# Optimization experiments

Hardware: AMD Instinct MI355X
Metric: run time of the kernel (lower is better)

## Reference

```python
import jax, jax.numpy as jnp
import numpy as np

T, B, I, H = 2048, 2048, 1, 20


def setup_inputs() -> dict:
    key = jax.random.key(0)
    k0, k1, k2, k3, k4 = jax.random.split(key, 5)
    x = jax.random.normal(k0, (T, B, I), dtype=jnp.float32)
    # Concatenated gate weights in order [f, i, o, c]; equivalent to the
    # module's 8 separate nn.Linear layers (wf/uf, wi/ui, wo/uo, wc/uc).
    W = jax.random.normal(k1, (4 * H, I), dtype=jnp.float32) * 0.2
    U = jax.random.normal(k2, (4 * H, H), dtype=jnp.float32) * 0.2
    bw = jax.random.normal(k3, (4 * H,), dtype=jnp.float32) * 0.1  # Linear(w*) biases
    bu = jax.random.normal(k4, (4 * H,), dtype=jnp.float32) * 0.1  # Linear(u*) biases
    return {"x": x, "W": W, "U": U, "bw": bw, "bu": bu}


def reference(x, W, U, bw, bu):
    h_dim = U.shape[1]
    b = x.shape[1]
    # Precompute input projections for all timesteps: (T, B, 4H).
    # Original adds both Linear biases (bw from w*, bu from u*) plus zero b*.
    xz = jnp.einsum('tbi,gi->tbg', x, W) + bw + bu

    def step(carry, xz_t):
        h, c = carry
        z = xz_t + h @ U.T  # (B, 4H)
        f, i, o, g = jnp.split(z, 4, axis=-1)
        f = jax.nn.sigmoid(f)
        i = jax.nn.sigmoid(i)
        o = jax.nn.sigmoid(o)
        g = jnp.tanh(g)
        c = f * c + i * g
        h = o * jnp.tanh(c)
        return (h, c), h

    h0 = jnp.zeros((b, h_dim), dtype=x.dtype)
    c0 = jnp.zeros((b, h_dim), dtype=x.dtype)
    (h_last, c_last), h_seq = jax.lax.scan(step, (h0, c0), xz)
    return h_seq, h_last, c_last
```

## Files before the change

kernel.cpp:

```cpp
#include <hip/hip_runtime.h>
#include <cstddef>


constexpr int T = 2048;
constexpr int B = 2048;
constexpr int H = 20;
constexpr int GR = 3;
constexpr int SLOTS = 4;
constexpr int ROW = 36;
constexpr int CHUNK = 16;
constexpr int NCH = T / CHUNK;

typedef float f2   __attribute__((ext_vector_type(2)));
typedef float f4ma __attribute__((ext_vector_type(4), may_alias));

__device__ __forceinline__ float rcp_f(float v) { return __builtin_amdgcn_rcpf(v); }
__device__ __forceinline__ float ex2(float v)   { return __builtin_amdgcn_exp2f(v); }

__global__ __launch_bounds__(64, 1)
void lstm_w7(const float* __restrict__ xg, const float* __restrict__ Wg,
             const float* __restrict__ Ug, const float* __restrict__ bwg,
             const float* __restrict__ bug, float* __restrict__ out) {
  __shared__ float hx[2][SLOTS * ROW];

  const int tid = threadIdx.x;
  const int bl  = tid / H;
  const int j   = tid % H;
  const int bg0 = blockIdx.x * GR + bl;
  const bool st = (bl < GR) && (bg0 < B);
  const int bgi = (bg0 < B) ? bg0 : (B - 1);

  constexpr float K1 = 1.44269504f;

  f2 u01[H], u23[H], w01, w23, b01, b23;
#pragma unroll
  for (int k = 0; k < H; ++k) {
    u01[k].x = Ug[(0 * H + j) * H + k] * (-K1);
    u01[k].y = Ug[(1 * H + j) * H + k] * (-K1);
    u23[k].x = Ug[(2 * H + j) * H + k] * (-K1);
    u23[k].y = Ug[(3 * H + j) * H + k] * (2.0f * K1);
  }
  w01.x = Wg[0 * H + j] * (-K1);   w01.y = Wg[1 * H + j] * (-K1);
  w23.x = Wg[2 * H + j] * (-K1);   w23.y = Wg[3 * H + j] * (2.0f * K1);
  b01.x = (bwg[0 * H + j] + bug[0 * H + j]) * (-K1);
  b01.y = (bwg[1 * H + j] + bug[1 * H + j]) * (-K1);
  b23.x = (bwg[2 * H + j] + bug[2 * H + j]) * (-K1);
  b23.y = (bwg[3 * H + j] + bug[3 * H + j]) * (2.0f * K1);

  for (int q = tid; q < 2 * SLOTS * ROW; q += 64) (&hx[0][0])[q] = 0.f;
  __builtin_amdgcn_wave_barrier();

  float xv[CHUNK];
#pragma unroll
  for (int s = 0; s < CHUNK; ++s) xv[s] = xg[(size_t)s * B + bgi];

  float c2 = 0.f;
  float hn = 0.f;
  float* outp = out + (size_t)bgi * H + j;
  constexpr size_t OS = (size_t)B * H;

  const int hbase = bl * ROW;

  for (int ch = 0; ch < NCH; ++ch) {
#pragma unroll
    for (int s = 0; s < CHUNK; ++s) {
      const int p = s & 1;
      __builtin_amdgcn_wave_barrier();
      const f4ma* hp = reinterpret_cast<const f4ma*>(&hx[p][hbase]);
      const f4ma v0 = hp[0], v1 = hp[1], v2 = hp[2], v3 = hp[3], v4 = hp[4];
      const float hb[H] = {v0.x, v0.y, v0.z, v0.w, v1.x, v1.y, v1.z, v1.w,
                           v2.x, v2.y, v2.z, v2.w, v3.x, v3.y, v3.z, v3.w,
                           v4.x, v4.y, v4.z, v4.w};
      const float xu = xv[s];
      {
        int tp = (ch + 1) * CHUNK + s;
        tp = (tp < T) ? tp : (T - 1);
        xv[s] = xg[(size_t)tp * B + bgi];
      }
      f2 za01 = b01, za23 = b23;
      f2 zb01 = u01[10] * hb[10], zb23 = u23[10] * hb[10];
#pragma unroll
      for (int k = 0; k < 10; ++k) {
        za01 = u01[k] * hb[k] + za01;
        za23 = u23[k] * hb[k] + za23;
      }
#pragma unroll
      for (int k = 11; k < H; ++k) {
        zb01 = u01[k] * hb[k] + zb01;
        zb23 = u23[k] * hb[k] + zb23;
      }
      f2 xv2; xv2.x = xu; xv2.y = xu;
      const f2 z01 = w01 * xv2 + (za01 + zb01);
      const f2 z23 = w23 * xv2 + (za23 + zb23);
      const float fg = rcp_f(1.f + ex2(z01.x));
      const float ig = rcp_f(1.f + ex2(z01.y));
      const float og = rcp_f(1.f + ex2(z23.x));
      const float gt = fmaf(-2.f, rcp_f(1.f + ex2(z23.y)), 1.f);
      const float igt2 = (2.f * K1 * ig) * gt;
      c2 = fmaf(fg, c2, igt2);
      const float r = rcp_f(1.f + ex2(c2));
      hn = fmaf(-2.f * og, r, og);
      hx[p ^ 1][hbase + j] = hn;
      if (st) *outp = hn;
      outp += OS;
    }
  }

  if (st) {
    out[OS * T + (size_t)bg0 * H + j] = hn;
    out[OS * (T + 1) + (size_t)bg0 * H + j] = c2 * 0.34657359f;
  }
}

extern "C" void kernel_launch(void* const* d_in, const int* in_sizes, int n_in,
                              void* d_out, int out_size, void* d_ws, size_t ws_size,
                              hipStream_t stream) {
  (void)in_sizes; (void)n_in; (void)d_ws; (void)ws_size; (void)out_size;
  const float* x  = (const float*)d_in[0];
  const float* W  = (const float*)d_in[1];
  const float* U  = (const float*)d_in[2];
  const float* bw = (const float*)d_in[3];
  const float* bu = (const float*)d_in[4];
  float* out = (float*)d_out;

  const int grid = (B + GR - 1) / GR;
  lstm_w7<<<dim3(grid), dim3(64), 0, stream>>>(x, W, U, bw, bu, out);
}
```

Baseline: 549.8 us.

## Split gates across lane pairs with DPP exchange, one batch row per wave

Each wave now handles a single batch element. Each hidden unit is computed by two lanes that each own two gates, and the activations are exchanged with a DPP lane swap. This halves the per-lane recurrent dot-product work and splits the accumulation into four shorter chains, cutting the serial per-step latency. Input x values are staged through LDS with chunk double-buffering instead of per-lane register arrays. The cost is 2048 waves instead of about 683, plus extra DPP and select operations in every step.

```diff
diff --git a/kernel.cpp b/kernel.cpp
--- a/kernel.cpp
+++ b/kernel.cpp
@@ -5,9 +5,6 @@
 constexpr int T = 2048;
 constexpr int B = 2048;
 constexpr int H = 20;
-constexpr int GR = 3;
-constexpr int SLOTS = 4;
-constexpr int ROW = 36;
 constexpr int CHUNK = 16;
 constexpr int NCH = T / CHUNK;
 
@@ -16,99 +13,116 @@
 
 __device__ __forceinline__ float rcp_f(float v) { return __builtin_amdgcn_rcpf(v); }
 __device__ __forceinline__ float ex2(float v)   { return __builtin_amdgcn_exp2f(v); }
+__device__ __forceinline__ float dpp_swap1(float v) {
+  return __int_as_float(__builtin_amdgcn_update_dpp(
+      0, __float_as_int(v), 0xB1, 0xF, 0xF, true));
+}
 
 __global__ __launch_bounds__(64, 1)
-void lstm_w7(const float* __restrict__ xg, const float* __restrict__ Wg,
+void lstm_w8(const float* __restrict__ xg, const float* __restrict__ Wg,
              const float* __restrict__ Ug, const float* __restrict__ bwg,
              const float* __restrict__ bug, float* __restrict__ out) {
-  __shared__ float hx[2][SLOTS * ROW];
+  __shared__ float hx[2][64];
+  __shared__ float xl[2][CHUNK];
 
   const int tid = threadIdx.x;
-  const int bl  = tid / H;
-  const int j   = tid % H;
-  const int bg0 = blockIdx.x * GR + bl;
-  const bool st = (bl < GR) && (bg0 < B);
-  const int bgi = (bg0 < B) ? bg0 : (B - 1);
+  const int p   = tid & 1;
+  const int jr  = tid >> 1;
+  const int jc  = (jr < H) ? jr : (H - 1);
+  const int b   = blockIdx.x;
+  const bool st = (p == 0) && (jr < H);
 
   constexpr float K1 = 1.44269504f;
+  const float s0 = -K1;
+  const float s1 = p ? (2.f * K1) : -K1;
+  const int g0 = p ? 2 : 0;
+  const int g1 = p ? 3 : 1;
 
-  f2 u01[H], u23[H], w01, w23, b01, b23;
+  f2 u2[H];
 #pragma unroll
   for (int k = 0; k < H; ++k) {
-    u01[k].x = Ug[(0 * H + j) * H + k] * (-K1);
-    u01[k].y = Ug[(1 * H + j) * H + k] * (-K1);
-    u23[k].x = Ug[(2 * H + j) * H + k] * (-K1);
-    u23[k].y = Ug[(3 * H + j) * H + k] * (2.0f * K1);
+    u2[k].x = Ug[(g0 * H + jc) * H + k] * s0;
+    u2[k].y = Ug[(g1 * H + jc) * H + k] * s1;
   }
-  w01.x = Wg[0 * H + j] * (-K1);   w01.y = Wg[1 * H + j] * (-K1);
-  w23.x = Wg[2 * H + j] * (-K1);   w23.y = Wg[3 * H + j] * (2.0f * K1);
-  b01.x = (bwg[0 * H + j] + bug[0 * H + j]) * (-K1);
-  b01.y = (bwg[1 * H + j] + bug[1 * H + j]) * (-K1);
-  b23.x = (bwg[2 * H + j] + bug[2 * H + j]) * (-K1);
-  b23.y = (bwg[3 * H + j] + bug[3 * H + j]) * (2.0f * K1);
+  f2 w2, b2, A, Bv;
+  w2.x = Wg[g0 * H + jc] * s0;  w2.y = Wg[g1 * H + jc] * s1;
+  b2.x = (bwg[g0 * H + jc] + bug[g0 * H + jc]) * s0;
+  b2.y = (bwg[g1 * H + jc] + bug[g1 * H + jc]) * s1;
+  A.x = 1.f;  A.y = p ? -2.f : (2.f * K1);
+  Bv.x = 0.f; Bv.y = p ? 1.f : 0.f;
 
-  for (int q = tid; q < 2 * SLOTS * ROW; q += 64) (&hx[0][0])[q] = 0.f;
+  const int wslot = p ? (32 + jr) : jr;
+
+  for (int q = tid; q < 2 * 64; q += 64) (&hx[0][0])[q] = 0.f;
+  if (tid < 2 * CHUNK) (&xl[0][0])[tid] = 0.f;
   __builtin_amdgcn_wave_barrier();
 
-  float xv[CHUNK];
-#pragma unroll
-  for (int s = 0; s < CHUNK; ++s) xv[s] = xg[(size_t)s * B + bgi];
+  if (tid < CHUNK) xl[0][tid] = xg[(size_t)tid * B + b];
+  float xnext = (tid < CHUNK) ? xg[(size_t)(CHUNK + tid) * B + b] : 0.f;
+  __builtin_amdgcn_wave_barrier();
 
   float c2 = 0.f;
   float hn = 0.f;
-  float* outp = out + (size_t)bgi * H + j;
+  float* outp = out + (size_t)b * H + jc;
   constexpr size_t OS = (size_t)B * H;
 
-  const int hbase = bl * ROW;
-
   for (int ch = 0; ch < NCH; ++ch) {
+    const int cb = ch & 1;
+    if (tid < CHUNK) {
+      xl[cb ^ 1][tid] = xnext;
+      const int tp = (ch + 2) * CHUNK + tid;
+      xnext = (tp < T) ? xg[(size_t)tp * B + b] : 0.f;
+    }
 #pragma unroll
     for (int s = 0; s < CHUNK; ++s) {
-      const int p = s & 1;
+      const int P = s & 1;
       __builtin_amdgcn_wave_barrier();
-      const f4ma* hp = reinterpret_cast<const f4ma*>(&hx[p][hbase]);
+      const f4ma* hp = reinterpret_cast<const f4ma*>(&hx[P][0]);
       const f4ma v0 = hp[0], v1 = hp[1], v2 = hp[2], v3 = hp[3], v4 = hp[4];
+      const float xv = xl[cb][s];
       const float hb[H] = {v0.x, v0.y, v0.z, v0.w, v1.x, v1.y, v1.z, v1.w,
                            v2.x, v2.y, v2.z, v2.w, v3.x, v3.y, v3.z, v3.w,
                            v4.x, v4.y, v4.z, v4.w};
-      const float xu = xv[s];
-      {
-        int tp = (ch + 1) * CHUNK + s;
-        tp = (tp < T) ? tp : (T - 1);
-        xv[s] = xg[(size_t)tp * B + bgi];
-      }
-      f2 za01 = b01, za23 = b23;
-      f2 zb01 = u01[10] * hb[10], zb23 = u23[10] * hb[10];
+      f2 h5;  h5.x  = hb[5];  h5.y  = hb[5];
+      f2 h10; h10.x = hb[10]; h10.y = hb[10];
+      f2 h15; h15.x = hb[15]; h15.y = hb[15];
+      f2 qa = b2, qb = u2[5] * h5, qc = u2[10] * h10, qd = u2[15] * h15;
 #pragma unroll
-      for (int k = 0; k < 10; ++k) {
-        za01 = u01[k] * hb[k] + za01;
-        za23 = u23[k] * hb[k] + za23;
-      }
+      for (int k = 0; k < 5; ++k)   { f2 hk; hk.x = hb[k]; hk.y = hb[k];
+                                      qa = u2[k] * hk + qa; }
 #pragma unroll
-      for (int k = 11; k < H; ++k) {
-        zb01 = u01[k] * hb[k] + zb01;
-        zb23 = u23[k] * hb[k] + zb23;
-      }
-      f2 xv2; xv2.x = xu; xv2.y = xu;
-      const f2 z01 = w01 * xv2 + (za01 + zb01);
-      const f2 z23 = w23 * xv2 + (za23 + zb23);
-      const float fg = rcp_f(1.f + ex2(z01.x));
-      const float ig = rcp_f(1.f + ex2(z01.y));
-      const float og = rcp_f(1.f + ex2(z23.x));
-      const float gt = fmaf(-2.f, rcp_f(1.f + ex2(z23.y)), 1.f);
-      const float igt2 = (2.f * K1 * ig) * gt;
-      c2 = fmaf(fg, c2, igt2);
-      const float r = rcp_f(1.f + ex2(c2));
-      hn = fmaf(-2.f * og, r, og);
-      hx[p ^ 1][hbase + j] = hn;
+      for (int k = 6; k < 10; ++k)  { f2 hk; hk.x = hb[k]; hk.y = hb[k];
+                                      qb = u2[k] * hk + qb; }
+#pragma unroll
+      for (int k = 11; k < 15; ++k) { f2 hk; hk.x = hb[k]; hk.y = hb[k];
+                                      qc = u2[k] * hk + qc; }
+#pragma unroll
+      for (int k = 16; k < 20; ++k) { f2 hk; hk.x = hb[k]; hk.y = hb[k];
+                                      qd = u2[k] * hk + qd; }
+      f2 xv2; xv2.x = xv; xv2.y = xv;
+      const f2 z2 = w2 * xv2 + ((qa + qb) + (qc + qd));
+      f2 r;
+      r.x = rcp_f(1.f + ex2(z2.x));
+      r.y = rcp_f(1.f + ex2(z2.y));
+      const f2 act2 = A * r + Bv;
+      f2 oth;
+      oth.x = dpp_swap1(act2.x);
+      oth.y = dpp_swap1(act2.y);
+      const float fg  = p ? oth.x : act2.x;
+      const float og  = p ? act2.x : oth.x;
+      const float igt = act2.y * oth.y;
+      c2 = fmaf(fg, c2, igt);
+      const float r2 = rcp_f(1.f + ex2(c2));
+      hn = fmaf(-2.f * og, r2, og);
+      hx[P ^ 1][wslot] = hn;
       if (st) *outp = hn;
       outp += OS;
     }
   }
 
   if (st) {
-    out[OS * T + (size_t)bg0 * H + j] = hn;
-    out[OS * (T + 1) + (size_t)bg0 * H + j] = c2 * 0.34657359f;
+    out[OS * T + (size_t)b * H + jr] = hn;
+    out[OS * (T + 1) + (size_t)b * H + jr] = c2 * 0.34657359f;
   }
 }
 
@@ -123,6 +137,5 @@
   const float* bu = (const float*)d_in[4];
   float* out = (float*)d_out;
 
-  const int grid = (B + GR - 1) / GR;
-  lstm_w7<<<dim3(grid), dim3(64), 0, stream>>>(x, W, U, bw, bu, out);
+  lstm_w8<<<dim3(B), dim3(64), 0, stream>>>(x, W, U, bw, bu, out);
 }
```

New measurement: 530.2 us. 1.04x faster.

## Stage x chunks through LDS and use single-buffered h with inline-asm LDS access

Applied to the files above, without the earlier changes.

Replaces the per-step global prefetch of x into a 16-entry register array with a double-buffered LDS staging area. One lane per time step writes the next chunk, which cuts register pressure and global loads per lane. The h exchange buffer becomes single-buffered, read and written through inline ds_read_b128/ds_write_b32 with an explicit lgkmcnt wait, and the matvec is split into four independent accumulator chains to shorten the dependency chain. The design relies on in-order LDS execution within a wave, so reading and writing the same buffer without a barrier is correct only if that ordering holds.

```diff
diff --git a/kernel.cpp b/kernel.cpp
--- a/kernel.cpp
+++ b/kernel.cpp
@@ -1,5 +1,6 @@
 #include <hip/hip_runtime.h>
 #include <cstddef>
+#include <cstdint>
 
 
 constexpr int T = 2048;
@@ -11,17 +12,18 @@
 constexpr int CHUNK = 16;
 constexpr int NCH = T / CHUNK;
 
-typedef float f2   __attribute__((ext_vector_type(2)));
-typedef float f4ma __attribute__((ext_vector_type(4), may_alias));
+typedef float f2 __attribute__((ext_vector_type(2)));
+typedef float f4 __attribute__((ext_vector_type(4)));
 
 __device__ __forceinline__ float rcp_f(float v) { return __builtin_amdgcn_rcpf(v); }
 __device__ __forceinline__ float ex2(float v)   { return __builtin_amdgcn_exp2f(v); }
 
 __global__ __launch_bounds__(64, 1)
-void lstm_w7(const float* __restrict__ xg, const float* __restrict__ Wg,
-             const float* __restrict__ Ug, const float* __restrict__ bwg,
-             const float* __restrict__ bug, float* __restrict__ out) {
-  __shared__ float hx[2][SLOTS * ROW];
+void lstm_w10(const float* __restrict__ xg, const float* __restrict__ Wg,
+              const float* __restrict__ Ug, const float* __restrict__ bwg,
+              const float* __restrict__ bug, float* __restrict__ out) {
+  __shared__ __align__(16) float hx[SLOTS * ROW];
+  __shared__ __align__(16) float xl[2 * SLOTS * CHUNK];
 
   const int tid = threadIdx.x;
   const int bl  = tid / H;
@@ -47,60 +49,83 @@
   b23.x = (bwg[2 * H + j] + bug[2 * H + j]) * (-K1);
   b23.y = (bwg[3 * H + j] + bug[3 * H + j]) * (2.0f * K1);
 
-  for (int q = tid; q < 2 * SLOTS * ROW; q += 64) (&hx[0][0])[q] = 0.f;
-  __builtin_amdgcn_wave_barrier();
+  const uint32_t hrd = (uint32_t)(size_t)(&hx[bl * ROW]);
+  const uint32_t hwr = hrd + 4u * (uint32_t)j;
+  const uint32_t xb  = (uint32_t)(size_t)(&xl[0]) + 64u * (uint32_t)bl;
+  const uint32_t xwb = (uint32_t)(size_t)(&xl[0]) + 64u * (uint32_t)bl
+                       + 4u * (uint32_t)j;
 
-  float xv[CHUNK];
-#pragma unroll
-  for (int s = 0; s < CHUNK; ++s) xv[s] = xg[(size_t)s * B + bgi];
+  for (int q = tid; q < SLOTS * ROW; q += 64) hx[q] = 0.f;
+  for (int q = tid; q < 2 * SLOTS * CHUNK; q += 64) xl[q] = 0.f;
+  if (j < CHUNK) xl[0 * 64 + bl * 16 + j] = xg[(size_t)j * B + bgi];
+  float xnext = (j < CHUNK) ? xg[(size_t)(CHUNK + j) * B + bgi] : 0.f;
+  asm volatile("s_waitcnt lgkmcnt(0)" ::: "memory");
 
-  float c2 = 0.f;
-  float hn = 0.f;
+  float c2 = 0.f, hn = 0.f;
   float* outp = out + (size_t)bgi * H + j;
   constexpr size_t OS = (size_t)B * H;
 
-  const int hbase = bl * ROW;
-
   for (int ch = 0; ch < NCH; ++ch) {
+    const int cb = ch & 1;
+    const uint32_t xrd = xb + (uint32_t)(cb * 256);
+    if (j < CHUNK) {
+      const uint32_t xw = xwb + (uint32_t)((cb ^ 1) * 256);
+      asm volatile("ds_write_b32 %0, %1" :: "v"(xw), "v"(xnext));
+      const int tp = (ch + 2) * CHUNK + j;
+      xnext = (tp < T) ? xg[(size_t)tp * B + bgi] : 0.f;
+    }
 #pragma unroll
     for (int s = 0; s < CHUNK; ++s) {
-      const int p = s & 1;
-      __builtin_amdgcn_wave_barrier();
-      const f4ma* hp = reinterpret_cast<const f4ma*>(&hx[p][hbase]);
-      const f4ma v0 = hp[0], v1 = hp[1], v2 = hp[2], v3 = hp[3], v4 = hp[4];
+      f4 v0, v1, v2, v3, v4; float xvv;
+      asm volatile(
+        "ds_read_b128 %0, %6 offset:0\n\t"
+        "ds_read_b128 %1, %6 offset:16\n\t"
+        "ds_read_b128 %2, %6 offset:32\n\t"
+        "ds_read_b128 %3, %6 offset:48\n\t"
+        "ds_read_b128 %4, %6 offset:64\n\t"
+        "ds_read_b32  %5, %7 offset:%8\n\t"
+        "s_waitcnt lgkmcnt(0)"
+        : "=v"(v0), "=v"(v1), "=v"(v2), "=v"(v3), "=v"(v4), "=v"(xvv)
+        : "v"(hrd), "v"(xrd), "i"(4 * s));
+      __builtin_amdgcn_sched_barrier(0);
       const float hb[H] = {v0.x, v0.y, v0.z, v0.w, v1.x, v1.y, v1.z, v1.w,
                            v2.x, v2.y, v2.z, v2.w, v3.x, v3.y, v3.z, v3.w,
                            v4.x, v4.y, v4.z, v4.w};
-      const float xu = xv[s];
-      {
-        int tp = (ch + 1) * CHUNK + s;
-        tp = (tp < T) ? tp : (T - 1);
-        xv[s] = xg[(size_t)tp * B + bgi];
-      }
-      f2 za01 = b01, za23 = b23;
-      f2 zb01 = u01[10] * hb[10], zb23 = u23[10] * hb[10];
+      f2 qa01 = b01, qa23 = b23;
+      f2 h5;  h5.x  = hb[5];  h5.y  = hb[5];
+      f2 h10; h10.x = hb[10]; h10.y = hb[10];
+      f2 h15; h15.x = hb[15]; h15.y = hb[15];
+      f2 qb01 = u01[5]  * h5,  qb23 = u23[5]  * h5;
+      f2 qc01 = u01[10] * h10, qc23 = u23[10] * h10;
+      f2 qd01 = u01[15] * h15, qd23 = u23[15] * h15;
 #pragma unroll
-      for (int k = 0; k < 10; ++k) {
-        za01 = u01[k] * hb[k] + za01;
-        za23 = u23[k] * hb[k] + za23;
-      }
+      for (int k = 0; k < 5; ++k)   { f2 hk; hk.x = hb[k]; hk.y = hb[k];
+                                      qa01 = u01[k] * hk + qa01;
+                                      qa23 = u23[k] * hk + qa23; }
 #pragma unroll
-      for (int k = 11; k < H; ++k) {
-        zb01 = u01[k] * hb[k] + zb01;
-        zb23 = u23[k] * hb[k] + zb23;
-      }
-      f2 xv2; xv2.x = xu; xv2.y = xu;
-      const f2 z01 = w01 * xv2 + (za01 + zb01);
-      const f2 z23 = w23 * xv2 + (za23 + zb23);
+      for (int k = 6; k < 10; ++k)  { f2 hk; hk.x = hb[k]; hk.y = hb[k];
+                                      qb01 = u01[k] * hk + qb01;
+                                      qb23 = u23[k] * hk + qb23; }
+#pragma unroll
+      for (int k = 11; k < 15; ++k) { f2 hk; hk.x = hb[k]; hk.y = hb[k];
+                                      qc01 = u01[k] * hk + qc01;
+                                      qc23 = u23[k] * hk + qc23; }
+#pragma unroll
+      for (int k = 16; k < 20; ++k) { f2 hk; hk.x = hb[k]; hk.y = hb[k];
+                                      qd01 = u01[k] * hk + qd01;
+                                      qd23 = u23[k] * hk + qd23; }
+      f2 xv2; xv2.x = xvv; xv2.y = xvv;
+      const f2 z01 = w01 * xv2 + ((qa01 + qb01) + (qc01 + qd01));
+      const f2 z23 = w23 * xv2 + ((qa23 + qb23) + (qc23 + qd23));
       const float fg = rcp_f(1.f + ex2(z01.x));
       const float ig = rcp_f(1.f + ex2(z01.y));
       const float og = rcp_f(1.f + ex2(z23.x));
       const float gt = fmaf(-2.f, rcp_f(1.f + ex2(z23.y)), 1.f);
       const float igt2 = (2.f * K1 * ig) * gt;
       c2 = fmaf(fg, c2, igt2);
-      const float r = rcp_f(1.f + ex2(c2));
-      hn = fmaf(-2.f * og, r, og);
-      hx[p ^ 1][hbase + j] = hn;
+      const float r2 = rcp_f(1.f + ex2(c2));
+      hn = fmaf(-2.f * og, r2, og);
+      asm volatile("ds_write_b32 %0, %1" :: "v"(hwr), "v"(hn));
       if (st) *outp = hn;
       outp += OS;
     }
@@ -124,5 +149,5 @@
   float* out = (float*)d_out;
 
   const int grid = (B + GR - 1) / GR;
-  lstm_w7<<<dim3(grid), dim3(64), 0, stream>>>(x, W, U, bw, bu, out);
+  lstm_w10<<<dim3(grid), dim3(64), 0, stream>>>(x, W, U, bw, bu, out);
 }
```

Result: faster. 497.0 us (-9.6%).

## Pack four batch rows per wave and broadcast hidden state via DPP

Applied to the files above, without the earlier changes.

Reworks the thread mapping so each 16-lane group handles one batch row, with each lane owning hidden unit i plus one of units 16-19. The hidden state is exchanged through DPP lane permutations instead of LDS writes and reads, and U weights are pre-permuted to match the DPP order. Inputs x are staged per chunk in LDS with prefetching, and there are four rows per block instead of three, giving fewer blocks. Each lane now evaluates two cells' gates, lengthening the serial chain per step. In exchange, the LDS round trip on the recurrent critical path goes away.

```diff
diff --git a/kernel.cpp b/kernel.cpp
--- a/kernel.cpp
+++ b/kernel.cpp
@@ -5,110 +5,133 @@
 constexpr int T = 2048;
 constexpr int B = 2048;
 constexpr int H = 20;
-constexpr int GR = 3;
-constexpr int SLOTS = 4;
-constexpr int ROW = 36;
 constexpr int CHUNK = 16;
 constexpr int NCH = T / CHUNK;
 
-typedef float f2   __attribute__((ext_vector_type(2)));
-typedef float f4ma __attribute__((ext_vector_type(4), may_alias));
+typedef float f2 __attribute__((ext_vector_type(2)));
 
 __device__ __forceinline__ float rcp_f(float v) { return __builtin_amdgcn_rcpf(v); }
 __device__ __forceinline__ float ex2(float v)   { return __builtin_amdgcn_exp2f(v); }
+template <int CTRL>
+__device__ __forceinline__ float dpp_f(float v) {
+  return __int_as_float(__builtin_amdgcn_update_dpp(
+      0, __float_as_int(v), CTRL, 0xF, 0xF, true));
+}
+__device__ __forceinline__ f2 dup(float v) { f2 r; r.x = v; r.y = v; return r; }
 
 __global__ __launch_bounds__(64, 1)
-void lstm_w7(const float* __restrict__ xg, const float* __restrict__ Wg,
+void lstm_qb(const float* __restrict__ xg, const float* __restrict__ Wg,
              const float* __restrict__ Ug, const float* __restrict__ bwg,
              const float* __restrict__ bug, float* __restrict__ out) {
-  __shared__ float hx[2][SLOTS * ROW];
+  __shared__ float xl[2][4][16];
 
   const int tid = threadIdx.x;
-  const int bl  = tid / H;
-  const int j   = tid % H;
-  const int bg0 = blockIdx.x * GR + bl;
-  const bool st = (bl < GR) && (bg0 < B);
-  const int bgi = (bg0 < B) ? bg0 : (B - 1);
+  const int row = tid >> 4;
+  const int i   = tid & 15;
+  const int b   = blockIdx.x * 4 + row;
+  const int ux  = i;
+  const int uy  = 16 + (i & 3);
 
   constexpr float K1 = 1.44269504f;
+  const float sg[4] = {-K1, -K1, -K1, 2.f * K1};
+  const int M[16] = {0,1,2,3, 7,6,5,4, 15,14,13,12, 8,9,10,11};
 
-  f2 u01[H], u23[H], w01, w23, b01, b23;
+  f2 um[4][16], ue[4][4], wW[4], bb[4];
 #pragma unroll
-  for (int k = 0; k < H; ++k) {
-    u01[k].x = Ug[(0 * H + j) * H + k] * (-K1);
-    u01[k].y = Ug[(1 * H + j) * H + k] * (-K1);
-    u23[k].x = Ug[(2 * H + j) * H + k] * (-K1);
-    u23[k].y = Ug[(3 * H + j) * H + k] * (2.0f * K1);
+  for (int g = 0; g < 4; ++g) {
+#pragma unroll
+    for (int q = 0; q < 16; ++q) {
+      const int k = i ^ M[q];
+      um[g][q].x = Ug[(g * H + ux) * H + k] * sg[g];
+      um[g][q].y = Ug[(g * H + uy) * H + k] * sg[g];
+    }
+#pragma unroll
+    for (int q = 0; q < 4; ++q) {
+      const int k = 16 + ((i ^ q) & 3);
+      ue[g][q].x = Ug[(g * H + ux) * H + k] * sg[g];
+      ue[g][q].y = Ug[(g * H + uy) * H + k] * sg[g];
+    }
+    wW[g].x = Wg[g * H + ux] * sg[g];
+    wW[g].y = Wg[g * H + uy] * sg[g];
+    bb[g].x = (bwg[g * H + ux] + bug[g * H + ux]) * sg[g];
+    bb[g].y = (bwg[g * H + uy] + bug[g * H + uy]) * sg[g];
   }
-  w01.x = Wg[0 * H + j] * (-K1);   w01.y = Wg[1 * H + j] * (-K1);
-  w23.x = Wg[2 * H + j] * (-K1);   w23.y = Wg[3 * H + j] * (2.0f * K1);
-  b01.x = (bwg[0 * H + j] + bug[0 * H + j]) * (-K1);
-  b01.y = (bwg[1 * H + j] + bug[1 * H + j]) * (-K1);
-  b23.x = (bwg[2 * H + j] + bug[2 * H + j]) * (-K1);
-  b23.y = (bwg[3 * H + j] + bug[3 * H + j]) * (2.0f * K1);
 
-  for (int q = tid; q < 2 * SLOTS * ROW; q += 64) (&hx[0][0])[q] = 0.f;
+  xl[0][row][i] = xg[(size_t)i * B + b];
+  float xnext = xg[(size_t)(CHUNK + i) * B + b];
   __builtin_amdgcn_wave_barrier();
 
-  float xv[CHUNK];
-#pragma unroll
-  for (int s = 0; s < CHUNK; ++s) xv[s] = xg[(size_t)s * B + bgi];
-
-  float c2 = 0.f;
-  float hn = 0.f;
-  float* outp = out + (size_t)bgi * H + j;
+  float hxv = 0.f, hyv = 0.f;
+  float cx = 0.f, cy = 0.f;
   constexpr size_t OS = (size_t)B * H;
-
-  const int hbase = bl * ROW;
+  float* outx = out + (size_t)b * H + ux;
+  float* outy = out + (size_t)b * H + uy;
 
   for (int ch = 0; ch < NCH; ++ch) {
+    const int cb = ch & 1;
+    xl[cb ^ 1][row][i] = xnext;
+    { const int tp = (ch + 2) * CHUNK + i;
+      xnext = (tp < T) ? xg[(size_t)tp * B + b] : 0.f; }
 #pragma unroll
     for (int s = 0; s < CHUNK; ++s) {
-      const int p = s & 1;
       __builtin_amdgcn_wave_barrier();
-      const f4ma* hp = reinterpret_cast<const f4ma*>(&hx[p][hbase]);
-      const f4ma v0 = hp[0], v1 = hp[1], v2 = hp[2], v3 = hp[3], v4 = hp[4];
-      const float hb[H] = {v0.x, v0.y, v0.z, v0.w, v1.x, v1.y, v1.z, v1.w,
-                           v2.x, v2.y, v2.z, v2.w, v3.x, v3.y, v3.z, v3.w,
-                           v4.x, v4.y, v4.z, v4.w};
-      const float xu = xv[s];
+      float hx[16], hy[4];
+      hx[0] = hxv;
+      hx[1] = dpp_f<0xB1>(hxv);
+      hx[2] = dpp_f<0x4E>(hxv);
+      hx[3] = dpp_f<0x4E>(hx[1]);
+#pragma unroll
+      for (int q = 0; q < 4; ++q) hx[4 + q] = dpp_f<0x141>(hx[q]);
+#pragma unroll
+      for (int q = 0; q < 8; ++q) hx[8 + q] = dpp_f<0x140>(hx[q]);
+      hy[0] = hyv;
+      hy[1] = dpp_f<0xB1>(hyv);
+      hy[2] = dpp_f<0x4E>(hyv);
+      hy[3] = dpp_f<0x4E>(hy[1]);
+      const float xu = xl[cb][row][s];
+
+      f2 z[4];
+#pragma unroll
+      for (int g = 0; g < 4; ++g) {
+        f2 pA = bb[g];
+        f2 pB = wW[g] * dup(xu);
+#pragma unroll
+        for (int q = 0; q < 8; ++q)  pA = um[g][q] * dup(hx[q]) + pA;
+#pragma unroll
+        for (int q = 8; q < 16; ++q) pB = um[g][q] * dup(hx[q]) + pB;
+#pragma unroll
+        for (int q = 0; q < 4; ++q)  pB = ue[g][q] * dup(hy[q]) + pB;
+        z[g] = pA + pB;
+      }
       {
-        int tp = (ch + 1) * CHUNK + s;
-        tp = (tp < T) ? tp : (T - 1);
-        xv[s] = xg[(size_t)tp * B + bgi];
+        const float fg = rcp_f(1.f + ex2(z[0].x));
+        const float ig = rcp_f(1.f + ex2(z[1].x));
+        const float og = rcp_f(1.f + ex2(z[2].x));
+        const float gt = fmaf(-2.f, rcp_f(1.f + ex2(z[3].x)), 1.f);
+        cx = fmaf(fg, cx, (2.f * K1 * ig) * gt);
+        const float r2 = rcp_f(1.f + ex2(cx));
+        hxv = fmaf(-2.f * og, r2, og);
       }
-      f2 za01 = b01, za23 = b23;
-      f2 zb01 = u01[10] * hb[10], zb23 = u23[10] * hb[10];
-#pragma unroll
-      for (int k = 0; k < 10; ++k) {
-        za01 = u01[k] * hb[k] + za01;
-        za23 = u23[k] * hb[k] + za23;
+      {
+        const float fg = rcp_f(1.f + ex2(z[0].y));
+        const float ig = rcp_f(1.f + ex2(z[1].y));
+        const float og = rcp_f(1.f + ex2(z[2].y));
+        const float gt = fmaf(-2.f, rcp_f(1.f + ex2(z[3].y)), 1.f);
+        cy = fmaf(fg, cy, (2.f * K1 * ig) * gt);
+        const float r2 = rcp_f(1.f + ex2(cy));
+        hyv = fmaf(-2.f * og, r2, og);
       }
-#pragma unroll
-      for (int k = 11; k < H; ++k) {
-        zb01 = u01[k] * hb[k] + zb01;
-        zb23 = u23[k] * hb[k] + zb23;
-      }
-      f2 xv2; xv2.x = xu; xv2.y = xu;
-      const f2 z01 = w01 * xv2 + (za01 + zb01);
-      const f2 z23 = w23 * xv2 + (za23 + zb23);
-      const float fg = rcp_f(1.f + ex2(z01.x));
-      const float ig = rcp_f(1.f + ex2(z01.y));
-      const float og = rcp_f(1.f + ex2(z23.x));
-      const float gt = fmaf(-2.f, rcp_f(1.f + ex2(z23.y)), 1.f);
-      const float igt2 = (2.f * K1 * ig) * gt;
-      c2 = fmaf(fg, c2, igt2);
-      const float r = rcp_f(1.f + ex2(c2));
-      hn = fmaf(-2.f * og, r, og);
-      hx[p ^ 1][hbase + j] = hn;
-      if (st) *outp = hn;
-      outp += OS;
+      *outx = hxv;
+      if (i < 4) *outy = hyv;
+      outx += OS; outy += OS;
     }
   }
 
-  if (st) {
-    out[OS * T + (size_t)bg0 * H + j] = hn;
-    out[OS * (T + 1) + (size_t)bg0 * H + j] = c2 * 0.34657359f;
+  out[OS * T + (size_t)b * H + ux] = hxv;
+  out[OS * (T + 1) + (size_t)b * H + ux] = cx * 0.34657359f;
+  if (i < 4) {
+    out[OS * T + (size_t)b * H + uy] = hyv;
+    out[OS * (T + 1) + (size_t)b * H + uy] = cy * 0.34657359f;
   }
 }
 
@@ -123,6 +146,5 @@
   const float* bu = (const float*)d_in[4];
   float* out = (float*)d_out;
 
-  const int grid = (B + GR - 1) / GR;
-  lstm_w7<<<dim3(grid), dim3(64), 0, stream>>>(x, W, U, bw, bu, out);
+  lstm_qb<<<dim3(B / 4), dim3(64), 0, stream>>>(x, W, U, bw, bu, out);
 }
```

After: 777.0 us. 1.41x slower.
